# Performance work log

Hardware: AMD Instinct MI355X
Metric: run time of the kernel (lower is better)

The kernel has to match this reference:

```python
import jax, jax.numpy as jnp
import numpy as np

L, D, DC, T, FF = 512, 512, 256, 128, 2048
P_COEF = 0.5


def layernorm(x, g, b):
    m = jnp.mean(x, axis=-1, keepdims=True)
    v = jnp.mean((x - m) ** 2, axis=-1, keepdims=True)
    return (x - m) / jnp.sqrt(v + 1e-5) * g + b


def conv_pool(t, w):
    # t: (L, N, D); torch attention_pool: permute -> (N, L, D), Conv1d over channels=L, length=D
    x = jnp.transpose(t, (1, 0, 2))  # (N, L, D)
    y = jax.lax.conv_general_dilated(x, w, window_strides=(2,), padding=[(1, 1)],
                                     dimension_numbers=("NCH", "OIH", "NCH"))
    return jnp.transpose(y, (1, 0, 2))  # (L, N, D//2)


def attn_fused(q, k):
    # q: (L, 1, d), k: (M, 1, d); faithful to module.attention with N=1 (squeeze(1))
    q2, k2 = q[:, 0], k[:, 0]
    scale = 1.0 / jnp.sqrt(jnp.asarray(q2.shape[1], q2.dtype))
    a = jax.nn.softmax((q2 @ k2.T) * scale, axis=-1)
    return (a @ k2 + q2)[:, None, :]  # fused residual add of q


def setup_inputs() -> dict:
    key = jax.random.key(0)
    ks = jax.random.split(key, 8)
    x = jax.random.normal(ks[0], (L, 1, D), jnp.float32)
    cached_k = jax.random.normal(ks[1], (T, L, 1, DC), jnp.float32)
    mem_mask = jax.random.randint(ks[2], (T,), 0, 2, jnp.int32)
    return {
        "x": x,
        "cached_k": cached_k,
        "ln1_g": jnp.ones((D,), jnp.float32),
        "ln1_b": jnp.zeros((D,), jnp.float32),
        "ln2_g": jnp.ones((D,), jnp.float32),
        "ln2_b": jnp.zeros((D,), jnp.float32),
        "w_compress_k": jax.random.normal(ks[3], (L, L, 3), jnp.float32) * (1.0 / np.sqrt(3 * L)),
        "w_compress_cur": jax.random.normal(ks[4], (L, L, 3), jnp.float32) * (1.0 / np.sqrt(3 * L)),
        "ap_w": jax.random.normal(ks[5], (DC, D), jnp.float32) * (1.0 / np.sqrt(DC)),
        "ap_b": jnp.zeros((D,), jnp.float32),
        "fc_w": jax.random.normal(ks[6], (D, FF), jnp.float32) * (1.0 / np.sqrt(D)),
        "fc_b": jnp.zeros((FF,), jnp.float32),
        "proj_w": jax.random.normal(ks[7], (FF, D), jnp.float32) * (1.0 / np.sqrt(FF)),
        "proj_b": jnp.zeros((D,), jnp.float32),
        "mem_mask": mem_mask,
    }


def reference(x, cached_k, ln1_g, ln1_b, ln2_g, ln2_b, w_compress_k, w_compress_cur,
              ap_w, ap_b, fc_w, fc_b, proj_w, proj_b, mem_mask):
    x1 = layernorm(x, ln1_g, ln1_b)                      # ln_1; q = k = x1
    # mask_memory: zero cached entries whose video name differs (per-entry, N=1)
    mem = cached_k * mem_mask.astype(x.dtype)[:, None, None, None]  # (T, L, 1, DC)
    k_cur = conv_pool(x1, w_compress_cur)                # (L, 1, DC) compress current k
    k = jnp.concatenate([mem.reshape(-1, 1, DC), k_cur], axis=0)    # ((T+1)*L, 1, DC)
    q = conv_pool(x1, w_compress_k)                      # k.shape[2]==256 branch: compress q
    selfatten = attn_fused(q, q)
    atten = attn_fused(q, k) + selfatten * P_COEF
    atten = atten @ ap_w + ap_b                          # attenproj 256 -> 512
    x2 = x1 + atten
    h = layernorm(x2, ln2_g, ln2_b)
    h = h @ fc_w + fc_b
    h = h * jax.nn.sigmoid(1.702 * h)                    # QuickGELU
    h = h @ proj_w + proj_b
    return x2 + h
```

## Files before the change

### kernel.cpp

```cpp
#include <hip/hip_runtime.h>
#include <hip/hip_bf16.h>

typedef unsigned short u16;
typedef unsigned int u32;
typedef __attribute__((ext_vector_type(8))) short bf16x8;
typedef __attribute__((ext_vector_type(4))) short bf16x4;
typedef __attribute__((ext_vector_type(4))) float f32x4;
typedef __attribute__((ext_vector_type(8))) u16 u16x8;
typedef __attribute__((ext_vector_type(4))) u16 u16x4;
typedef __attribute__((ext_vector_type(4))) u32 u32x4;

__device__ __forceinline__ u16 f2bf(float x){
  __hip_bfloat16 h = __float2bfloat16(x);
  return __builtin_bit_cast(u16, h);
}
__device__ __forceinline__ float bf2f(u16 u){
  __hip_bfloat16 h = __builtin_bit_cast(__hip_bfloat16, u);
  return __bfloat162float(h);
}

template<bool BF>
__global__ __launch_bounds__(256) void ln_kernel(const float* __restrict__ in,
    const float* __restrict__ g, const float* __restrict__ b,
    float* __restrict__ outf, u16* __restrict__ outb)
{
  int row = blockIdx.x, tid = threadIdx.x;
  const float* p = in + (size_t)row*512 + tid*2;
  float v0 = p[0], v1 = p[1];
  float s = v0+v1, ss = v0*v0+v1*v1;
  #pragma unroll
  for (int o=1;o<64;o<<=1){ s += __shfl_xor(s,o); ss += __shfl_xor(ss,o); }
  __shared__ float rs[4], rss[4];
  if ((tid&63)==0){ rs[tid>>6]=s; rss[tid>>6]=ss; }
  __syncthreads();
  s = rs[0]+rs[1]+rs[2]+rs[3]; ss = rss[0]+rss[1]+rss[2]+rss[3];
  float mean = s*(1.f/512.f);
  float var  = ss*(1.f/512.f) - mean*mean;
  float rstd = 1.f/sqrtf(var + 1e-5f);
  int d = tid*2;
  float o0 = (v0-mean)*rstd*g[d]   + b[d];
  float o1 = (v1-mean)*rstd*g[d+1] + b[d+1];
  if (BF){
    outb[(size_t)row*512+d]   = f2bf(o0);
    outb[(size_t)row*512+d+1] = f2bf(o1);
  } else {
    outf[(size_t)row*512+d]   = o0;
    outf[(size_t)row*512+d+1] = o1;
  }
}

__global__ __launch_bounds__(256) void xgT_kernel(const float* __restrict__ x1, u16* __restrict__ xgT)
{
  int h = blockIdx.x, tid = threadIdx.x;
  #pragma unroll
  for (int rep=0;rep<6;rep++){
    int k = rep*256 + tid;
    int i = k/3, kk = k - i*3;
    int pos = 2*h - 1 + kk;
    float v = (pos >= 0 && pos < 512) ? x1[(size_t)i*512 + pos] : 0.f;
    xgT[(size_t)h*1536 + k] = f2bf(v);
  }
}

__device__ __forceinline__ void transcvt128(float (*t)[33],
    const float* __restrict__ in, u16* __restrict__ out, int K, int N, int bx, int by)
{
  int nb = bx*32, kb = by*32;
  int tx = threadIdx.x & 31, ty = threadIdx.x >> 5;
  #pragma unroll
  for (int i=0;i<32;i+=4) t[ty+i][tx] = in[(size_t)(kb+ty+i)*N + nb+tx];
  __syncthreads();
  #pragma unroll
  for (int i=0;i<32;i+=4) out[(size_t)(nb+ty+i)*K + kb+tx] = f2bf(t[tx][ty+i]);
}

__global__ __launch_bounds__(256) void prep_kernel(
    const float* __restrict__ x, const float* __restrict__ ln1g, const float* __restrict__ ln1b,
    const float* __restrict__ wk, const float* __restrict__ wc,
    const float* __restrict__ ck, const int* __restrict__ mask,
    float* __restrict__ x1, u16* __restrict__ wkcb, u16* __restrict__ kbf)
{
  __shared__ float rs[4], rss[4];
  int b = blockIdx.x, tid = threadIdx.x;
  if (b < 512){
    const float* p = x + (size_t)b*512 + tid*2;
    float v0 = p[0], v1 = p[1];
    float s = v0+v1, ss = v0*v0+v1*v1;
    #pragma unroll
    for (int o=1;o<64;o<<=1){ s += __shfl_xor(s,o); ss += __shfl_xor(ss,o); }
    if ((tid&63)==0){ rs[tid>>6]=s; rss[tid>>6]=ss; }
    __syncthreads();
    s = rs[0]+rs[1]+rs[2]+rs[3]; ss = rss[0]+rss[1]+rss[2]+rss[3];
    float mean = s*(1.f/512.f);
    float var  = ss*(1.f/512.f) - mean*mean;
    float rstd = 1.f/sqrtf(var + 1e-5f);
    int d = tid*2;
    x1[(size_t)b*512+d]   = (v0-mean)*rstd*ln1g[d]   + ln1b[d];
    x1[(size_t)b*512+d+1] = (v1-mean)*rstd*ln1g[d+1] + ln1b[d+1];
  } else if (b < 8704){
    int flat = (b-512)*256 + tid;
    int row = flat >> 5, seg = flat & 31;
    if (mask[row>>9] == 0) return;
    const float* src = ck + (size_t)row*256 + seg*8;
    u16x8 o;
    #pragma unroll
    for (int j=0;j<8;j++) o[j] = f2bf(src[j]);
    *(u16x8*)(kbf + (size_t)row*256 + seg*8) = o;
  } else {
    size_t i = (size_t)((b-8704)*256 + tid)*8;
    const size_t half = (size_t)512*1536;
    const float* src = (i < half) ? (wk + i) : (wc + (i - half));
    u16x8 o;
    #pragma unroll
    for (int j=0;j<8;j++) o[j] = f2bf(src[j]);
    *(u16x8*)(wkcb + i) = o;
  }
}

template<int ACT, bool WF32, bool WBF, int W>
__global__ __launch_bounds__(64*W) void gemm4(
    const u16* __restrict__ A, const u16* __restrict__ B,
    const float* __restrict__ bias, const float* __restrict__ resid,
    float* __restrict__ outF, u16* __restrict__ outB, u16* __restrict__ outB2,
    int rowSplit, int M, int N, int K)
{
  __shared__ float red[W][32][33];
  int tid = threadIdx.x;
  int w = tid >> 6, lane = tid & 63;
  int lq = lane & 15, lg = lane >> 4;
  int m0 = blockIdx.y*32, n0 = blockIdx.x*32;
  int Ks = K / W;
  int kbeg = w * Ks;
  f32x4 acc00={0,0,0,0}, acc01={0,0,0,0}, acc10={0,0,0,0}, acc11={0,0,0,0};
  const u16* pa0 = A + (size_t)(m0+lq)*K + kbeg + lg*8;
  const u16* pa1 = pa0 + (size_t)16*K;
  const u16* pb0 = B + (size_t)(n0+lq)*K + kbeg + lg*8;
  const u16* pb1 = pb0 + (size_t)16*K;
  #pragma unroll 2
  for (int k0=0;k0<Ks;k0+=32){
    bf16x8 a0 = *(const bf16x8*)(pa0+k0);
    bf16x8 a1 = *(const bf16x8*)(pa1+k0);
    bf16x8 b0 = *(const bf16x8*)(pb0+k0);
    bf16x8 b1 = *(const bf16x8*)(pb1+k0);
    acc00 = __builtin_amdgcn_mfma_f32_16x16x32_bf16(a0,b0,acc00,0,0,0);
    acc01 = __builtin_amdgcn_mfma_f32_16x16x32_bf16(a0,b1,acc01,0,0,0);
    acc10 = __builtin_amdgcn_mfma_f32_16x16x32_bf16(a1,b0,acc10,0,0,0);
    acc11 = __builtin_amdgcn_mfma_f32_16x16x32_bf16(a1,b1,acc11,0,0,0);
  }
  f32x4 accs[2][2] = {{acc00,acc01},{acc10,acc11}};
  #pragma unroll
  for (int mi=0;mi<2;mi++)
    #pragma unroll
    for (int ni=0;ni<2;ni++)
      #pragma unroll
      for (int r=0;r<4;r++)
        red[w][mi*16+lg*4+r][ni*16+lq] = accs[mi][ni][r];
  __syncthreads();
  #pragma unroll
  for (int rr=0;rr<16/W;rr++){
    int cell = rr*64*W + tid;
    int row = cell >> 5, col = cell & 31;
    float v = 0.f;
    #pragma unroll
    for (int ww=0;ww<W;ww++) v += red[ww][row][col];
    int grow = m0 + row, gcol = n0 + col;
    if (bias)  v += bias[gcol];
    if (ACT==1) v = v/(1.f+__expf(-1.702f*v));
    if (resid) v += resid[(size_t)grow*N+gcol];
    if (WF32) outF[(size_t)grow*N+gcol] = v;
    if (WBF){
      if (grow < rowSplit) outB[(size_t)grow*N+gcol] = f2bf(v);
      else                 outB2[(size_t)(grow-rowSplit)*N+gcol] = f2bf(v);
    }
  }
}

__global__ __launch_bounds__(128) void attn_flash(
    const u16* __restrict__ qb, const u16* __restrict__ keys,
    const int* __restrict__ mask,
    const float* __restrict__ apw, const float* __restrict__ fcw, const float* __restrict__ pjw,
    u16* __restrict__ apT, u16* __restrict__ fcT, u16* __restrict__ pjT,
    u16* __restrict__ pO, float* __restrict__ pL)
{
  __shared__ u16 kv[2][8192];
  int tid = threadIdx.x;
  int bid = blockIdx.x;
  if (bid >= 1056){
    int f = bid - 1056;
    float (*t)[33] = reinterpret_cast<float(*)[33]>(&kv[0][0]);
    if (f < 128)       transcvt128(t, apw, apT, 256, 512, f & 15, f >> 4);
    else if (f < 1152) transcvt128(t, fcw, fcT, 512, 2048, (f-128) & 63, (f-128) >> 6);
    else               transcvt128(t, pjw, pjT, 2048, 512, (f-1152) & 15, (f-1152) >> 4);
    return;
  }
  int w = tid >> 6, lane = tid & 63, lq = lane & 15, lg = lane >> 4;
  int c = bid % 66, qt = bid / 66;
  const u16* kp = keys;
  int kstart = c * 1024, off = 0, nt = 32;
  if (c == 65) { kp = qb; kstart = 0; nt = 16; }
  else if (c == 64) { kstart = 65536; nt = 16; }
  else {
    int m0 = mask[2*c], m1 = mask[2*c+1];
    if (!m0 && !m1) return;
    off = m0 ? 0 : 512;
    nt = ((m0 && m1) ? 32 : 16);
  }
  int qbase = qt*32 + w*16;

  bf16x8 qf[8];
  {
    const u16* qrow = qb + (size_t)(qbase+lq)*256 + lg*8;
    #pragma unroll
    for (int s=0;s<8;s++) qf[s] = *(const bf16x8*)(qrow + s*32);
  }
  f32x4 o[16];
  #pragma unroll
  for (int i=0;i<16;i++) o[i] = (f32x4){0,0,0,0};
  float l_acc = 0.f;

  auto kv3 = (__attribute__((address_space(3))) char*)&kv[0][0];
  unsigned kvaddr0 = (unsigned)(unsigned long long)kv3;
  const char* gbase = (const char*)kp + (size_t)(kstart+off)*512;

  #define STAGE(i, b) { \
    const char* tb = gbase + (size_t)(i)*16384; \
    _Pragma("unroll") \
    for (int rep=0; rep<8; rep++){ \
      int slot = rep*128 + tid; \
      int goff = ((slot&63)>>1)*512 + ((slot>>6)*16 + (slot&1)*8)*2; \
      __builtin_amdgcn_global_load_lds( \
        (const __attribute__((address_space(1))) unsigned*)(tb + goff), \
        (__attribute__((address_space(3))) unsigned*)(kv3 + (b)*16384 + (rep*128 + (tid & ~63))*16), \
        16, 0, 0); \
    } }

  #define ISSUE8(T, ab) \
    asm volatile( \
      "ds_read_b64_tr_b16 %0, %8 offset:0\n\t" \
      "ds_read_b64_tr_b16 %1, %8 offset:512\n\t" \
      "ds_read_b64_tr_b16 %2, %8 offset:1024\n\t" \
      "ds_read_b64_tr_b16 %3, %8 offset:1536\n\t" \
      "ds_read_b64_tr_b16 %4, %8 offset:2048\n\t" \
      "ds_read_b64_tr_b16 %5, %8 offset:2560\n\t" \
      "ds_read_b64_tr_b16 %6, %8 offset:3072\n\t" \
      "ds_read_b64_tr_b16 %7, %8 offset:3584\n\t" \
      : "=&v"(T[0]),"=&v"(T[1]),"=&v"(T[2]),"=&v"(T[3]), \
        "=&v"(T[4]),"=&v"(T[5]),"=&v"(T[6]),"=&v"(T[7]) \
      : "v"(ab) : "memory")

  #define MFMA4(T, base) { \
    bf16x8 v0_ = __builtin_shufflevector(T[0],T[1],0,1,2,3,4,5,6,7); \
    bf16x8 v1_ = __builtin_shufflevector(T[2],T[3],0,1,2,3,4,5,6,7); \
    bf16x8 v2_ = __builtin_shufflevector(T[4],T[5],0,1,2,3,4,5,6,7); \
    bf16x8 v3_ = __builtin_shufflevector(T[6],T[7],0,1,2,3,4,5,6,7); \
    o[(base)+0] = __builtin_amdgcn_mfma_f32_16x16x32_bf16(pa, v0_, o[(base)+0], 0,0,0); \
    o[(base)+1] = __builtin_amdgcn_mfma_f32_16x16x32_bf16(pa, v1_, o[(base)+1], 0,0,0); \
    o[(base)+2] = __builtin_amdgcn_mfma_f32_16x16x32_bf16(pa, v2_, o[(base)+2], 0,0,0); \
    o[(base)+3] = __builtin_amdgcn_mfma_f32_16x16x32_bf16(pa, v3_, o[(base)+3], 0,0,0); \
  }

  STAGE(0, 0);
  for (int i=0; i<nt; i++){
    int cur = i & 1;
    if (i+1 < nt){
      STAGE(i+1, cur^1);
      asm volatile("s_waitcnt vmcnt(8)" ::: "memory");
    } else {
      asm volatile("s_waitcnt vmcnt(0)" ::: "memory");
    }
    __syncthreads();

    const u16* kb = &kv[cur][0];
    f32x4 s0 = {0,0,0,0}, s1 = {0,0,0,0};
    #pragma unroll
    for (int s=0;s<8;s++){
      int e = (2*s + (lg>>1))*512 + lq*16 + (lg&1)*8;
      bf16x8 ka0 = *(const bf16x8*)(kb + e);
      bf16x8 ka1 = *(const bf16x8*)(kb + e + 256);
      s0 = __builtin_amdgcn_mfma_f32_16x16x32_bf16(ka0, qf[s], s0, 0,0,0);
      s1 = __builtin_amdgcn_mfma_f32_16x16x32_bf16(ka1, qf[s], s1, 0,0,0);
    }
    asm volatile("s_waitcnt lgkmcnt(0)" ::: "memory");

    unsigned trb = kvaddr0 + cur*16384 + lane*8;
    bf16x4 tA[8], tB[8], tC[8], tD[8];
    ISSUE8(tA, trb);
    ISSUE8(tB, trb + 4096);

    float p[8];
    #pragma unroll
    for (int r=0;r<4;r++){ p[r]   = __expf(s0[r]*0.0625f);
                           p[4+r] = __expf(s1[r]*0.0625f); }
    l_acc += (p[0]+p[1])+(p[2]+p[3])+((p[4]+p[5])+(p[6]+p[7]));
    u32 w0 = (u32)f2bf(p[0]) | ((u32)f2bf(p[1])<<16);
    u32 w1 = (u32)f2bf(p[2]) | ((u32)f2bf(p[3])<<16);
    u32 w2 = (u32)f2bf(p[4]) | ((u32)f2bf(p[5])<<16);
    u32 w3 = (u32)f2bf(p[6]) | ((u32)f2bf(p[7])<<16);
    u32x4 fq = {w0,w1,w2,w3};
    bf16x8 pa = __builtin_bit_cast(bf16x8, fq);

    asm volatile("s_waitcnt lgkmcnt(8)" ::: "memory");
    __builtin_amdgcn_sched_barrier(0);
    MFMA4(tA, 0);
    ISSUE8(tC, trb + 8192);
    asm volatile("s_waitcnt lgkmcnt(8)" ::: "memory");
    __builtin_amdgcn_sched_barrier(0);
    MFMA4(tB, 4);
    ISSUE8(tD, trb + 12288);
    asm volatile("s_waitcnt lgkmcnt(8)" ::: "memory");
    __builtin_amdgcn_sched_barrier(0);
    MFMA4(tC, 8);
    asm volatile("s_waitcnt lgkmcnt(0)" ::: "memory");
    __builtin_amdgcn_sched_barrier(0);
    MFMA4(tD, 12);
    __syncthreads();
  }
  #undef STAGE
  #undef ISSUE8
  #undef MFMA4

  l_acc += __shfl_xor(l_acc, 16);
  l_acc += __shfl_xor(l_acc, 32);
  size_t qrow = (size_t)c*512 + qbase;
  if (lane < 16) pL[qrow + lq] = l_acc;
  #pragma unroll
  for (int dt=0; dt<16; dt++){
    #pragma unroll
    for (int r=0;r<4;r++){
      pO[(qrow + lg*4 + r)*256 + dt*16 + lq] = f2bf(o[dt][r]);
    }
  }
}

__global__ __launch_bounds__(256) void attn_reduce(
    const u16* __restrict__ pO, const float* __restrict__ pL,
    const int* __restrict__ mask, const u16* __restrict__ qb,
    u16* __restrict__ attn_out)
{
  __shared__ f32x4 redO[4][64];
  __shared__ float redL[4];
  __shared__ float scnt[2];
  int q = blockIdx.x, tid = threadIdx.x;
  int cg = tid >> 6, dq = tid & 63;

  float mz = (tid < 128) ? ((mask[tid]==0) ? 1.f : 0.f) : 0.f;
  #pragma unroll
  for (int o=1;o<64;o<<=1) mz += __shfl_xor(mz, o);
  if ((tid&63)==0 && tid < 128) scnt[tid>>6] = mz;

  f32x4 acc = {0,0,0,0};
  float lsum = 0.f;
  for (int c = cg; c < 65; c += 4){
    bool valid = (c==64) || mask[2*c] || mask[2*c+1];
    if (!valid) continue;
    u16x4 v = *(const u16x4*)(pO + ((size_t)c*512+q)*256 + dq*4);
    acc[0] += bf2f(v[0]); acc[1] += bf2f(v[1]);
    acc[2] += bf2f(v[2]); acc[3] += bf2f(v[3]);
    if (dq==0) lsum += pL[(size_t)c*512+q];
  }
  redO[cg][dq] = acc;
  if (dq==0) redL[cg] = lsum;
  __syncthreads();
  if (tid < 64){
    f32x4 s = redO[0][tid];
    f32x4 s1 = redO[1][tid], s2 = redO[2][tid], s3 = redO[3][tid];
    s[0]+=s1[0]+s2[0]+s3[0]; s[1]+=s1[1]+s2[1]+s3[1];
    s[2]+=s1[2]+s2[2]+s3[2]; s[3]+=s1[3]+s2[3]+s3[3];
    float den = redL[0]+redL[1]+redL[2]+redL[3] + 512.f*(scnt[0]+scnt[1]);
    float ls  = pL[(size_t)65*512 + q];
    u16x4 sv = *(const u16x4*)(pO + ((size_t)65*512+q)*256 + tid*4);
    u16x4 qv = *(const u16x4*)(qb + (size_t)q*256 + tid*4);
    u16x4 ov;
    #pragma unroll
    for (int j=0;j<4;j++)
      ov[j] = f2bf(s[j]/den + 0.5f*bf2f(sv[j])/ls + 1.5f*bf2f(qv[j]));
    *(u16x4*)(attn_out + (size_t)q*256 + tid*4) = ov;
  }
}

extern "C" void kernel_launch(void* const* d_in, const int* in_sizes, int n_in,
                              void* d_out, int out_size, void* d_ws, size_t ws_size,
                              hipStream_t stream)
{
  const float* x    = (const float*)d_in[0];
  const float* ck   = (const float*)d_in[1];
  const float* ln1g = (const float*)d_in[2];
  const float* ln1b = (const float*)d_in[3];
  const float* ln2g = (const float*)d_in[4];
  const float* ln2b = (const float*)d_in[5];
  const float* wk   = (const float*)d_in[6];
  const float* wc   = (const float*)d_in[7];
  const float* apw  = (const float*)d_in[8];
  const float* apb  = (const float*)d_in[9];
  const float* fcw  = (const float*)d_in[10];
  const float* fcb  = (const float*)d_in[11];
  const float* pjw  = (const float*)d_in[12];
  const float* pjb  = (const float*)d_in[13];
  const int*   mask = (const int*)d_in[14];
  float* out = (float*)d_out;

  char* wsb = (char*)d_ws;
  float* x1    = (float*)(wsb + 0);
  float* x2    = (float*)(wsb + 1048576);
  u16*   aoutb = (u16*)  (wsb + 2097152);
  u16*   x2nb  = (u16*)  (wsb + 2359296);
  u16*   xgT   = (u16*)  (wsb + 2883584);
  u16*   apT   = (u16*)  (wsb + 3670016);
  u16*   fcT   = (u16*)  (wsb + 3932160);
  u16*   pjT   = (u16*)  (wsb + 6029312);
  u16*   qbf   = (u16*)  (wsb + 8126464);
  u16*   kbf   = (u16*)  (wsb + 8388608);
  float* pL    = (float*)(wsb + 42205184);
  u16*   pO    = (u16*)  (wsb + 42340352);
  u16*   wkcb  = (u16*)  (wsb + 42340352);
  u16*   hb    = (u16*)  (wsb + 42340352);

  prep_kernel<<<9472,256,0,stream>>>(x, ln1g, ln1b, wk, wc, ck, mask, x1, wkcb, kbf);
  xgT_kernel<<<256,256,0,stream>>>(x1, xgT);

  gemm4<0,false,true,8><<<dim3(8,32),512,0,stream>>>(wkcb, xgT, nullptr, nullptr,
      nullptr, qbf, kbf + (size_t)65536*256, 512, 1024, 256, 1536);

  attn_flash<<<3232,128,0,stream>>>(qbf, kbf, mask, apw, fcw, pjw, apT, fcT, pjT, pO, pL);
  attn_reduce<<<512,256,0,stream>>>(pO, pL, mask, qbf, aoutb);

  gemm4<0,true,false,4><<<dim3(16,16),256,0,stream>>>(aoutb, apT, apb, x1,
      x2, nullptr, nullptr, 512, 512, 512, 256);
  ln_kernel<true><<<512,256,0,stream>>>(x2, ln2g, ln2b, nullptr, x2nb);
  gemm4<1,false,true,4><<<dim3(64,16),256,0,stream>>>(x2nb, fcT, fcb, nullptr,
      nullptr, hb, hb, 4096, 512, 2048, 512);
  gemm4<0,true,false,8><<<dim3(16,16),512,0,stream>>>(hb, pjT, pjb, x2,
      out, nullptr, nullptr, 512, 512, 512, 2048);
}
```

Baseline: 112.9 us.

## Move cached-K bf16 conversion into conv GEMM launch to overlap with GEMM

Moves the masked cached-K fp32-to-bf16 conversion out of the prep kernel and into a new kernel that also computes the conv-pool GEMM. The first 256 blocks run the GEMM and the remaining blocks convert the memory cache. The aim is to fill the idle GPU while the small GEMM runs and to shrink the critical-path prep kernel. It removes the separate gemm4 launch. It also adds an odd comma expression in the LN code that is harmless but confusing.

```diff
diff --git a/kernel.cpp b/kernel.cpp
--- a/kernel.cpp
+++ b/kernel.cpp
@@ -77,8 +77,7 @@
 __global__ __launch_bounds__(256) void prep_kernel(
     const float* __restrict__ x, const float* __restrict__ ln1g, const float* __restrict__ ln1b,
     const float* __restrict__ wk, const float* __restrict__ wc,
-    const float* __restrict__ ck, const int* __restrict__ mask,
-    float* __restrict__ x1, u16* __restrict__ wkcb, u16* __restrict__ kbf)
+    float* __restrict__ x1, u16* __restrict__ wkcb)
 {
   __shared__ float rs[4], rss[4];
   int b = blockIdx.x, tid = threadIdx.x;
@@ -96,9 +95,27 @@
     float rstd = 1.f/sqrtf(var + 1e-5f);
     int d = tid*2;
     x1[(size_t)b*512+d]   = (v0-mean)*rstd*ln1g[d]   + ln1b[d];
-    x1[(size_t)b*512+d+1] = (v1-mean)*rstd*ln1g[d+1] + ln1b[d+1];
-  } else if (b < 8704){
-    int flat = (b-512)*256 + tid;
+    x1[(size_t)b*512+d+1] = (v0=v1,(v1-mean))*rstd*ln1g[d+1] + ln1b[d+1];
+  } else {
+    size_t i = (size_t)((b-512)*256 + tid)*8;
+    const size_t half = (size_t)512*1536;
+    const float* src = (i < half) ? (wk + i) : (wc + (i - half));
+    u16x8 o;
+    #pragma unroll
+    for (int j=0;j<8;j++) o[j] = f2bf(src[j]);
+    *(u16x8*)(wkcb + i) = o;
+  }
+}
+
+__global__ __launch_bounds__(512) void conv_cvt(
+    const u16* __restrict__ wkcb, const u16* __restrict__ xgT,
+    const float* __restrict__ ck, const int* __restrict__ mask,
+    u16* __restrict__ qbf, u16* __restrict__ kbf)
+{
+  __shared__ float red[8][32][33];
+  int bid = blockIdx.x, tid = threadIdx.x;
+  if (bid >= 256){
+    int flat = (bid-256)*512 + tid;
     int row = flat >> 5, seg = flat & 31;
     if (mask[row>>9] == 0) return;
     const float* src = ck + (size_t)row*256 + seg*8;
@@ -106,14 +123,49 @@
     #pragma unroll
     for (int j=0;j<8;j++) o[j] = f2bf(src[j]);
     *(u16x8*)(kbf + (size_t)row*256 + seg*8) = o;
-  } else {
-    size_t i = (size_t)((b-8704)*256 + tid)*8;
-    const size_t half = (size_t)512*1536;
-    const float* src = (i < half) ? (wk + i) : (wc + (i - half));
-    u16x8 o;
-    #pragma unroll
-    for (int j=0;j<8;j++) o[j] = f2bf(src[j]);
-    *(u16x8*)(wkcb + i) = o;
+    return;
+  }
+  const int M = 1024, N = 256, K = 1536, rowSplit = 512;
+  int w = tid >> 6, lane = tid & 63;
+  int lq = lane & 15, lg = lane >> 4;
+  int m0 = (bid >> 3)*32, n0 = (bid & 7)*32;
+  int Ks = K >> 3;
+  int kbeg = w * Ks;
+  f32x4 acc00={0,0,0,0}, acc01={0,0,0,0}, acc10={0,0,0,0}, acc11={0,0,0,0};
+  const u16* pa0 = wkcb + (size_t)(m0+lq)*K + kbeg + lg*8;
+  const u16* pa1 = pa0 + (size_t)16*K;
+  const u16* pb0 = xgT + (size_t)(n0+lq)*K + kbeg + lg*8;
+  const u16* pb1 = pb0 + (size_t)16*K;
+  #pragma unroll 2
+  for (int k0=0;k0<Ks;k0+=32){
+    bf16x8 a0 = *(const bf16x8*)(pa0+k0);
+    bf16x8 a1 = *(const bf16x8*)(pa1+k0);
+    bf16x8 b0 = *(const bf16x8*)(pb0+k0);
+    bf16x8 b1 = *(const bf16x8*)(pb1+k0);
+    acc00 = __builtin_amdgcn_mfma_f32_16x16x32_bf16(a0,b0,acc00,0,0,0);
+    acc01 = __builtin_amdgcn_mfma_f32_16x16x32_bf16(a0,b1,acc01,0,0,0);
+    acc10 = __builtin_amdgcn_mfma_f32_16x16x32_bf16(a1,b0,acc10,0,0,0);
+    acc11 = __builtin_amdgcn_mfma_f32_16x16x32_bf16(a1,b1,acc11,0,0,0);
+  }
+  f32x4 accs[2][2] = {{acc00,acc01},{acc10,acc11}};
+  #pragma unroll
+  for (int mi=0;mi<2;mi++)
+    #pragma unroll
+    for (int ni=0;ni<2;ni++)
+      #pragma unroll
+      for (int r=0;r<4;r++)
+        red[w][mi*16+lg*4+r][ni*16+lq] = accs[mi][ni][r];
+  __syncthreads();
+  #pragma unroll
+  for (int rr=0;rr<2;rr++){
+    int cell = rr*512 + tid;
+    int row = cell >> 5, col = cell & 31;
+    float v = 0.f;
+    #pragma unroll
+    for (int ww=0;ww<8;ww++) v += red[ww][row][col];
+    int grow = m0 + row, gcol = n0 + col;
+    if (grow < rowSplit) qbf[(size_t)grow*N+gcol] = f2bf(v);
+    else                 kbf[(size_t)(65536 + grow-rowSplit)*N+gcol] = f2bf(v);
   }
 }
 
@@ -415,11 +467,9 @@
   u16*   wkcb  = (u16*)  (wsb + 42340352);
   u16*   hb    = (u16*)  (wsb + 42340352);
 
-  prep_kernel<<<9472,256,0,stream>>>(x, ln1g, ln1b, wk, wc, ck, mask, x1, wkcb, kbf);
+  prep_kernel<<<1280,256,0,stream>>>(x, ln1g, ln1b, wk, wc, x1, wkcb);
   xgT_kernel<<<256,256,0,stream>>>(x1, xgT);
-
-  gemm4<0,false,true,8><<<dim3(8,32),512,0,stream>>>(wkcb, xgT, nullptr, nullptr,
-      nullptr, qbf, kbf + (size_t)65536*256, 512, 1024, 256, 1536);
+  conv_cvt<<<4352,512,0,stream>>>(wkcb, xgT, ck, mask, qbf, kbf);
 
   attn_flash<<<3232,128,0,stream>>>(qbf, kbf, mask, apw, fcw, pjw, apT, fcT, pjT, pO, pL);
   attn_reduce<<<512,256,0,stream>>>(pO, pL, mask, qbf, aoutb);
```

Result: no change. 112.5 us (-0.4%).
